# Kernel tuning notes

Measured on AMD Instinct MI355X. Metric: run time of the kernel, lower is better.

The kernel has to match this reference:

```python
import jax, jax.numpy as jnp
import numpy as np

BETA = 0.25


def setup_inputs() -> dict:
    key = jax.random.key(0)
    k1, k2 = jax.random.split(key)
    x = jax.random.normal(k1, (32, 64, 64, 64), dtype=jnp.float32)   # [B, C, H, W]
    emb = jax.random.normal(k2, (1024, 64), dtype=jnp.float32)       # [K, C] codebook
    return {"x": x, "emb": emb}


def reference(x, emb):
    b, c, h, w = x.shape
    # (b h w) c
    z = jnp.transpose(x, (0, 2, 3, 1)).reshape(-1, c)
    # squared euclidean distances (argmin identical to torch.cdist argmin)
    # ||z||^2 - 2 z e^T + ||e||^2, never taking sqrt since only argmin is used
    d = (jnp.sum(z * z, axis=1, keepdims=True)
         - 2.0 * jnp.einsum('nc,kc->nk', z, emb)
         + jnp.sum(emb * emb, axis=1)[None, :])        # [N, K]
    idx = jnp.argmin(d, axis=1)                        # [N] int
    e = emb[idx]                                       # gather [N, C]
    e = jnp.transpose(e.reshape(b, h, w, c), (0, 3, 1, 2))  # [B, C, H, W]
    codebook_loss = jnp.mean((jax.lax.stop_gradient(x) - e) ** 2)
    commitment_loss = BETA * jnp.mean((x - jax.lax.stop_gradient(e)) ** 2)
    loss = codebook_loss + commitment_loss
    o = x + jax.lax.stop_gradient(e - x)               # straight-through
    indices = idx.reshape(b, h, w)
    return (o, loss, indices)
```

## Files before the change

kernel.cpp:

```cpp
#include <hip/hip_runtime.h>

#define BATCH   32
#define CCH     64
#define HW      4096
#define NPIX    (BATCH * HW)
#define KCODES  1024
#define NELEM   (NPIX * CCH)
#define MB      256
#define CK      64
#define MARGIN_Q 3u

typedef _Float16 f16;
typedef __attribute__((ext_vector_type(8))) _Float16 f16x8;
typedef __attribute__((ext_vector_type(4))) float    f32x4;

static __device__ __forceinline__ f32x4 mfma16(f16x8 a, f16x8 b, f32x4 c) {
    return __builtin_amdgcn_mfma_f32_16x16x32_f16(a, b, c, 0, 0, 0);
}

static __device__ __forceinline__ void dma16(void* lds, const void* g) {
    __builtin_amdgcn_global_load_lds(
        (const __attribute__((address_space(1))) unsigned int*)g,
        (__attribute__((address_space(3))) unsigned int*)lds, 16, 0, 0);
}

static __device__ __forceinline__ unsigned med3u(unsigned a, unsigned b, unsigned c) {
    unsigned d;
    asm("v_med3_u32 %0, %1, %2, %3" : "=v"(d) : "v"(a), "v"(b), "v"(c));
    return d;
}

#define WS_EEB_F   64
#define WS_CBH_B   8192
#define WS_CBL_B   139264
#define WS_WL_U    67584

__global__ __launch_bounds__(256) void vq_prep(
    const float* __restrict__ emb, float* __restrict__ wsf,
    unsigned* __restrict__ wsu, f16* __restrict__ cbH, f16* __restrict__ cbL,
    float* __restrict__ eeb_g)
{
    const int t   = threadIdx.x;
    const int gid = blockIdx.x * 256 + t;
    const int row = gid >> 3, gi = gid & 7;
    if (gid == 0) { wsf[0] = 0.f; wsu[1] = 0u; wsu[2] = 0u; }
    const float* src = emb + (size_t)row * CCH + gi * 8;
    float4 v0 = *(const float4*)(src);
    float4 v1 = *(const float4*)(src + 4);
    float vv[8] = {v0.x, v0.y, v0.z, v0.w, v1.x, v1.y, v1.z, v1.w};
    f16x8 h, l;
    float s = 0.f;
#pragma unroll
    for (int j = 0; j < 8; ++j) {
        f16 hh = (f16)vv[j];
        h[j] = hh;
        l[j] = (f16)(vv[j] - (float)hh);
        s = fmaf(vv[j], vv[j], s);
    }
    const int off = row * 64 + 8 * (gi ^ (row & 7));
    *(f16x8*)(cbH + off) = h;
    *(f16x8*)(cbL + off) = l;
    s += __shfl_xor(s, 1, 64);
    s += __shfl_xor(s, 2, 64);
    s += __shfl_xor(s, 4, 64);
    if (gi == 0) eeb_g[row] = fmaf(s, 2048.0f, 1048576.0f);
}

__global__ __launch_bounds__(512, 4) void vq_main(
    const float* __restrict__ x,
    const float* __restrict__ emb,
    const f16* __restrict__ cbH, const f16* __restrict__ cbL,
    const float* __restrict__ eeb_g,
    float* __restrict__ o, float* __restrict__ idx_out,
    float* __restrict__ acc, unsigned* __restrict__ wl_count,
    unsigned* __restrict__ wl, unsigned cap)
{
    __shared__ __align__(16) char smem[32768];
    __shared__ float eebl[2][CK];
    __shared__ unsigned bu1[MB], bu2[MB];
    __shared__ float wred[8];

    const int t    = threadIdx.x;
    const int lane = t & 63;
    const int w    = t >> 6;
    const int col  = lane & 15;
    const int quad = lane >> 4;
    const int c7   = col & 7;
    const int sw0  = 8 * (quad ^ c7);
    const int sw1  = sw0 ^ 32;
    const int n0   = blockIdx.x * MB;
    const int b    = n0 >> 12;
    const int p0   = n0 & 4095;
    const float* xb = x + (size_t)b * (CCH * HW) + p0;

    auto stage = [&](int chunk, int bufi) {
        const int k0 = chunk * CK;
        char* lb = smem + bufi * 16384;
        const char* gH = (const char*)cbH + (size_t)k0 * 128 + w * 1024 + lane * 16;
        const char* gL = (const char*)cbL + (size_t)k0 * 128 + w * 1024 + lane * 16;
        dma16(lb + w * 1024,        gH);
        dma16(lb + 8192 + w * 1024, gL);
        if (t < CK) eebl[bufi][t] = eeb_g[k0 + t];
    };

    stage(0, 0);

    f16x8 aH[2][2], aL[2][2];
#pragma unroll
    for (int rt = 0; rt < 2; ++rt) {
        const int pp = w * 32 + rt * 16 + col;
#pragma unroll
        for (int kc = 0; kc < 2; ++kc) {
            f16x8 h, l;
#pragma unroll
            for (int j = 0; j < 8; ++j) {
                const int c = kc * 32 + quad * 8 + j;
                float zs = -2.0f * xb[(size_t)c * HW + pp];
                f16 hh = (f16)zs;
                h[j] = hh;
                l[j] = (f16)(zs - (float)hh);
            }
            aH[rt][kc] = h;
            aL[rt][kc] = l;
        }
    }

    unsigned best[8], best2[8];
#pragma unroll
    for (int s = 0; s < 8; ++s) { best[s] = 0xFFFFFFFFu; best2[s] = 0xFFFFFFFFu; }

    const f32x4 zero4 = {0.f, 0.f, 0.f, 0.f};

    for (int chunk = 0; chunk < KCODES / CK; ++chunk) {
        const int cur = chunk & 1;
        __syncthreads();
        if (chunk + 1 < KCODES / CK) stage(chunk + 1, cur ^ 1);

        const f16* bufH = (const f16*)(smem + cur * 16384);
        const f16* bufL = bufH + 4096;
        const int k0 = chunk * CK;

#pragma unroll
        for (int tile = 0; tile < CK / 16; ++tile) {
            const f16* bh = bufH + (tile * 16 + col) * 64;
            const f16* bl = bufL + (tile * 16 + col) * 64;
            f16x8 bH0 = *(const f16x8*)(bh + sw0);
            f16x8 bH1 = *(const f16x8*)(bh + sw1);
            f16x8 bL0 = *(const f16x8*)(bl + sw0);
            f16x8 bL1 = *(const f16x8*)(bl + sw1);
            const float eebc = eebl[cur][tile * 16 + col];
            const unsigned kb = (unsigned)(k0 + tile * 16 + col);
#pragma unroll
            for (int rt = 0; rt < 2; ++rt) {
                f32x4 a4 = mfma16(aH[rt][0], bH0, zero4);
                a4 = mfma16(aH[rt][1], bH1, a4);
                a4 = mfma16(aL[rt][0], bH0, a4);
                a4 = mfma16(aL[rt][1], bH1, a4);
                a4 = mfma16(aH[rt][0], bL0, a4);
                a4 = mfma16(aH[rt][1], bL1, a4);
#pragma unroll
                for (int r = 0; r < 4; ++r) {
                    float uf = fmaf(a4[r], 2048.0f, eebc);
                    unsigned pk = (((unsigned)uf) << 10) | kb;
                    const int s = rt * 4 + r;
                    const unsigned b0 = best[s];
                    best2[s] = med3u(b0, best2[s], pk);
                    best[s]  = min(b0, pk);
                }
            }
        }
    }

#pragma unroll
    for (int d = 1; d < 16; d <<= 1) {
#pragma unroll
        for (int s = 0; s < 8; ++s) {
            unsigned ob  = __shfl_xor(best[s],  d, 64);
            unsigned ob2 = __shfl_xor(best2[s], d, 64);
            best2[s] = min(min(best2[s], ob2), max(best[s], ob));
            best[s]  = min(best[s], ob);
        }
    }
    if (col == 0) {
#pragma unroll
        for (int rt = 0; rt < 2; ++rt)
#pragma unroll
            for (int r = 0; r < 4; ++r) {
                const int pl = w * 32 + rt * 16 + quad * 4 + r;
                bu1[pl] = best[rt * 4 + r];
                bu2[pl] = best2[rt * 4 + r];
            }
    }
    __syncthreads();

    const int pix  = t & 255;
    const int half = t >> 8;
    const unsigned bu = bu1[pix];
    const unsigned bidx = bu & 1023u;
    if (half == 0) {
        idx_out[n0 + t] = (float)bidx;
        const unsigned qg = (bu2[pix] >> 10) - (bu >> 10);
        if (qg < MARGIN_Q) {
            unsigned pos = atomicAdd(wl_count, 1u);
            if (pos < cap) wl[pos] = (unsigned)(n0 + t);
        }
    }
    float ss = 0.f;
    {
        const float4* er4 = (const float4*)(emb + (size_t)bidx * CCH) + half * 8;
        const float* xbt = xb + pix;
        float* ob = o + (size_t)b * (CCH * HW) + p0 + pix;
#pragma unroll
        for (int i = 0; i < 8; ++i) {
            float4 ev = er4[i];
            float evv[4] = {ev.x, ev.y, ev.z, ev.w};
#pragma unroll
            for (int q = 0; q < 4; ++q) {
                const int c = half * 32 + i * 4 + q;
                float xv = xbt[(size_t)c * HW];
                float e  = evv[q];
                ob[(size_t)c * HW] = xv + (e - xv);
                float d = xv - e;
                ss = fmaf(d, d, ss);
            }
        }
    }
    for (int off = 32; off; off >>= 1) ss += __shfl_down(ss, off, 64);
    if (lane == 0) wred[w] = ss;
    __syncthreads();
    if (t == 0) {
        float s2 = 0.f;
#pragma unroll
        for (int q = 0; q < 8; ++q) s2 += wred[q];
        atomicAdd(acc, s2);
    }
}

__global__ __launch_bounds__(256) void vq_refine(
    const float* __restrict__ x, const float* __restrict__ emb,
    float* __restrict__ o, float* __restrict__ idx_out,
    float* __restrict__ acc, const unsigned* __restrict__ wl_count,
    const unsigned* __restrict__ wl, unsigned cap,
    float* __restrict__ loss, unsigned* __restrict__ done)
{
    __shared__ float zsh[CCH];
    __shared__ double rbd[4];
    __shared__ int rbi[4];
    __shared__ int s_pk;
    unsigned cnt = *wl_count; if (cnt > cap) cnt = cap;
    const int t = threadIdx.x;

    for (unsigned i = blockIdx.x; i < cnt; i += gridDim.x) {
        const int n = (int)wl[i];
        const int b = n >> 12, p = n & 4095;
        if (t < CCH) zsh[t] = x[(size_t)b * (CCH * HW) + (size_t)t * HW + p];
        __syncthreads();

        double bd = 1e300; int bi = KCODES;
        for (int j = 0; j < 4; ++j) {
            const int k = t + j * 256;
            const float* er = emb + (size_t)k * CCH;
            double d = 0.0;
#pragma unroll
            for (int c = 0; c < CCH; ++c) {
                double tt = (double)zsh[c] - (double)er[c];
                d = fma(tt, tt, d);
            }
            if (d < bd) { bd = d; bi = k; }
        }
        for (int dlt = 1; dlt < 64; dlt <<= 1) {
            double od = __shfl_xor(bd, dlt, 64);
            int    oi = __shfl_xor(bi, dlt, 64);
            if (od < bd || (od == bd && oi < bi)) { bd = od; bi = oi; }
        }
        const int wv = t >> 6;
        if ((t & 63) == 0) { rbd[wv] = bd; rbi[wv] = bi; }
        __syncthreads();
        if (t == 0) {
            double fb = rbd[0]; int fi = rbi[0];
            for (int q = 1; q < 4; ++q)
                if (rbd[q] < fb || (rbd[q] == fb && rbi[q] < fi)) { fb = rbd[q]; fi = rbi[q]; }
            const int old = (int)idx_out[n];
            if (fi != old) { idx_out[n] = (float)fi; s_pk = (old << 16) | fi; }
            else s_pk = -1;
        }
        __syncthreads();
        const int pk = s_pk;
        if (pk >= 0 && t < CCH) {
            const int old = pk >> 16, fi = pk & 0xFFFF;
            const float xv = zsh[t];
            const float eo = emb[(size_t)old * CCH + t];
            const float en = emb[(size_t)fi  * CCH + t];
            o[(size_t)b * (CCH * HW) + (size_t)t * HW + p] = xv + (en - xv);
            const float dn = xv - en, dd = xv - eo;
            float delta = dn * dn - dd * dd;
            for (int off = 32; off; off >>= 1) delta += __shfl_down(delta, off, 64);
            if (t == 0) atomicAdd(acc, delta);
        }
        __syncthreads();
    }

    __threadfence();
    if (t == 0) {
        unsigned prev = atomicAdd(done, 1u);
        if (prev + 1 == gridDim.x) {
            __threadfence();
            float a = atomicAdd(acc, 0.0f);
            loss[0] = 1.25f * a * (1.0f / (float)NELEM);
        }
    }
}

extern "C" void kernel_launch(void* const* d_in, const int* in_sizes, int n_in,
                              void* d_out, int out_size, void* d_ws, size_t ws_size,
                              hipStream_t stream) {
    const float* x   = (const float*)d_in[0];
    const float* emb = (const float*)d_in[1];
    float*    out = (float*)d_out;
    float*    wsf = (float*)d_ws;
    unsigned* wsu = (unsigned*)d_ws;
    char*     wsb = (char*)d_ws;

    float* o_out    = out;
    float* loss_out = out + NELEM;
    float* idx_out  = out + NELEM + 1;
    float* eeb_g    = wsf + WS_EEB_F;
    f16*   cbH      = (f16*)(wsb + WS_CBH_B);
    f16*   cbL      = (f16*)(wsb + WS_CBL_B);
    unsigned* wl    = wsu + WS_WL_U;
    unsigned cap = 0;
    if (ws_size / 4 > WS_WL_U) {
        size_t c = ws_size / 4 - WS_WL_U;
        cap = (unsigned)(c > NPIX ? NPIX : c);
    }

    vq_prep<<<32, 256, 0, stream>>>(emb, wsf, wsu, cbH, cbL, eeb_g);
    vq_main<<<NPIX / MB, 512, 0, stream>>>(x, emb, cbH, cbL, eeb_g, o_out,
                                           idx_out, wsf, wsu + 1, wl, cap);
    vq_refine<<<512, 256, 0, stream>>>(x, emb, o_out, idx_out, wsf,
                                       wsu + 1, wl, cap, loss_out, wsu + 2);
}
```

Measured before the change: 175.6 us.

## Double codebook chunk size, split MFMA chains, move loss finalization to separate kernel

The codebook staging chunk grows from 64 to 128 codes, which halves the number of barrier-separated iterations and doubles LDS use to 64KB plus extras. The six-MFMA dependent chain is split into two independent accumulators that are summed at the end, which shortens dependency latency. The last-block atomic completion counter in refine is replaced by a tiny separate finalize kernel, which adds one launch. The idx/worklist indexing is also fixed to use pix. The larger LDS footprint may reduce blocks per CU below the launch-bounds target of 4.

Measured after the change: 153.7 us. 1.14x faster.

```diff
diff --git a/kernel.cpp b/kernel.cpp
--- a/kernel.cpp
+++ b/kernel.cpp
@@ -7,7 +7,7 @@
 #define KCODES  1024
 #define NELEM   (NPIX * CCH)
 #define MB      256
-#define CK      64
+#define CK      128
 #define MARGIN_Q 3u
 
 typedef _Float16 f16;
@@ -43,7 +43,7 @@
     const int t   = threadIdx.x;
     const int gid = blockIdx.x * 256 + t;
     const int row = gid >> 3, gi = gid & 7;
-    if (gid == 0) { wsf[0] = 0.f; wsu[1] = 0u; wsu[2] = 0u; }
+    if (gid == 0) { wsf[0] = 0.f; wsu[1] = 0u; }
     const float* src = emb + (size_t)row * CCH + gi * 8;
     float4 v0 = *(const float4*)(src);
     float4 v1 = *(const float4*)(src + 4);
@@ -75,7 +75,7 @@
     float* __restrict__ acc, unsigned* __restrict__ wl_count,
     unsigned* __restrict__ wl, unsigned cap)
 {
-    __shared__ __align__(16) char smem[32768];
+    __shared__ __align__(16) char smem[65536];
     __shared__ float eebl[2][CK];
     __shared__ unsigned bu1[MB], bu2[MB];
     __shared__ float wred[8];
@@ -95,11 +95,15 @@
 
     auto stage = [&](int chunk, int bufi) {
         const int k0 = chunk * CK;
-        char* lb = smem + bufi * 16384;
-        const char* gH = (const char*)cbH + (size_t)k0 * 128 + w * 1024 + lane * 16;
-        const char* gL = (const char*)cbL + (size_t)k0 * 128 + w * 1024 + lane * 16;
-        dma16(lb + w * 1024,        gH);
-        dma16(lb + 8192 + w * 1024, gL);
+        char* lb = smem + bufi * 32768;
+        const char* gH = (const char*)cbH + (size_t)k0 * 128 + w * 2048 + lane * 16;
+        const char* gL = (const char*)cbL + (size_t)k0 * 128 + w * 2048 + lane * 16;
+        char* lH = lb + w * 2048;
+        char* lL = lb + 16384 + w * 2048;
+        dma16(lH,        gH);
+        dma16(lH + 1024, gH + 1024);
+        dma16(lL,        gL);
+        dma16(lL + 1024, gL + 1024);
         if (t < CK) eebl[bufi][t] = eeb_g[k0 + t];
     };
 
@@ -136,8 +140,8 @@
         __syncthreads();
         if (chunk + 1 < KCODES / CK) stage(chunk + 1, cur ^ 1);
 
-        const f16* bufH = (const f16*)(smem + cur * 16384);
-        const f16* bufL = bufH + 4096;
+        const f16* bufH = (const f16*)(smem + cur * 32768);
+        const f16* bufL = bufH + 8192;
         const int k0 = chunk * CK;
 
 #pragma unroll
@@ -152,15 +156,15 @@
             const unsigned kb = (unsigned)(k0 + tile * 16 + col);
 #pragma unroll
             for (int rt = 0; rt < 2; ++rt) {
-                f32x4 a4 = mfma16(aH[rt][0], bH0, zero4);
-                a4 = mfma16(aH[rt][1], bH1, a4);
-                a4 = mfma16(aL[rt][0], bH0, a4);
-                a4 = mfma16(aL[rt][1], bH1, a4);
-                a4 = mfma16(aH[rt][0], bL0, a4);
-                a4 = mfma16(aH[rt][1], bL1, a4);
+                f32x4 u = mfma16(aH[rt][0], bH0, zero4);
+                f32x4 v = mfma16(aH[rt][1], bH1, zero4);
+                u = mfma16(aL[rt][0], bH0, u);
+                v = mfma16(aL[rt][1], bH1, v);
+                u = mfma16(aH[rt][0], bL0, u);
+                v = mfma16(aH[rt][1], bL1, v);
 #pragma unroll
                 for (int r = 0; r < 4; ++r) {
-                    float uf = fmaf(a4[r], 2048.0f, eebc);
+                    float uf = fmaf(u[r] + v[r], 2048.0f, eebc);
                     unsigned pk = (((unsigned)uf) << 10) | kb;
                     const int s = rt * 4 + r;
                     const unsigned b0 = best[s];
@@ -198,11 +202,11 @@
     const unsigned bu = bu1[pix];
     const unsigned bidx = bu & 1023u;
     if (half == 0) {
-        idx_out[n0 + t] = (float)bidx;
+        idx_out[n0 + pix] = (float)bidx;
         const unsigned qg = (bu2[pix] >> 10) - (bu >> 10);
         if (qg < MARGIN_Q) {
             unsigned pos = atomicAdd(wl_count, 1u);
-            if (pos < cap) wl[pos] = (unsigned)(n0 + t);
+            if (pos < cap) wl[pos] = (unsigned)(n0 + pix);
         }
     }
     float ss = 0.f;
@@ -240,8 +244,7 @@
     const float* __restrict__ x, const float* __restrict__ emb,
     float* __restrict__ o, float* __restrict__ idx_out,
     float* __restrict__ acc, const unsigned* __restrict__ wl_count,
-    const unsigned* __restrict__ wl, unsigned cap,
-    float* __restrict__ loss, unsigned* __restrict__ done)
+    const unsigned* __restrict__ wl, unsigned cap)
 {
     __shared__ float zsh[CCH];
     __shared__ double rbd[4];
@@ -299,16 +302,10 @@
         }
         __syncthreads();
     }
-
-    __threadfence();
-    if (t == 0) {
-        unsigned prev = atomicAdd(done, 1u);
-        if (prev + 1 == gridDim.x) {
-            __threadfence();
-            float a = atomicAdd(acc, 0.0f);
-            loss[0] = 1.25f * a * (1.0f / (float)NELEM);
-        }
-    }
+}
+
+__global__ void vq_fin(const float* __restrict__ acc, float* __restrict__ loss) {
+    *loss = 1.25f * (*acc) * (1.0f / (float)NELEM);
 }
 
 extern "C" void kernel_launch(void* const* d_in, const int* in_sizes, int n_in,
@@ -338,5 +335,6 @@
     vq_main<<<NPIX / MB, 512, 0, stream>>>(x, emb, cbH, cbL, eeb_g, o_out,
                                            idx_out, wsf, wsu + 1, wl, cap);
     vq_refine<<<512, 256, 0, stream>>>(x, emb, o_out, idx_out, wsf,
-                                       wsu + 1, wl, cap, loss_out, wsu + 2);
-}
+                                       wsu + 1, wl, cap);
+    vq_fin<<<1, 1, 0, stream>>>(wsf, loss_out);
+}
```
